# Kernel tuning notes

Hardware: AMD Instinct MI355X
Metric: run time of the kernel (lower is better)

## Reference

```python
import jax, jax.numpy as jnp
import numpy as np

# static architecture constants (match init_kwargs)
H, D, N_BASIS, MEM_LEN, QLEN = 16, 128, 1024, 512, 2048
RIDGE = 0.5
BASIS_SIGMAS = (0.005, 0.01)


def _gaussian_pdf(x, mu, sigma):
    return jnp.exp(-0.5 * ((x - mu) / sigma) ** 2) / (sigma * jnp.sqrt(2.0 * jnp.pi))


def _basis_params(n):
    # torch.meshgrid(linspace(0,1,n//2), sigmas, indexing='ij') then flatten
    m = jnp.linspace(0.0, 1.0, n // len(BASIS_SIGMAS)).astype(jnp.float32)
    mu = jnp.repeat(m, len(BASIS_SIGMAS))
    sigma = jnp.tile(jnp.asarray(BASIS_SIGMAS, jnp.float32), n // len(BASIS_SIGMAS))
    return mu, sigma


def _compute_G(l, b_mu, b_sigma, n):
    # padded linear positions on [-0.5+shift, 1.5-shift], l even -> 2l points
    shift = 1.0 / (2 * l)
    pos = jnp.linspace(-0.5 + shift, 1.5 - shift, 2 * l).astype(jnp.float32)
    F = _gaussian_pdf(pos[None, :], b_mu[:, None], b_sigma[:, None])  # [N, 2l]
    # G = F^T (F F^T + ridge I)^{-1}, then crop padding rows -> [l, N]
    G = jnp.linalg.solve(F @ F.T + RIDGE * jnp.eye(n, dtype=jnp.float32), F).T
    return G[l // 2: -(l // 2)]


def _forward(k, q, W_key, W_val, W_out, w_mu, w_sigma):
    d = H * D
    b_mu, b_sigma = _basis_params(N_BASIS)
    k = k[:, -512:, :]                                   # forward truncates memory
    l = k.shape[1]
    G = _compute_G(l, b_mu, b_sigma, N_BASIS)            # [l, N]
    # value_function: project signal onto basis coefficients B -> [1, N, d]
    B = jnp.einsum('bld,ln->bnd', k, G)
    keys = (B @ W_key.T).reshape(1, N_BASIS, H, D).transpose(0, 2, 1, 3)    # [1,H,N,D]
    values = (B @ W_val.T).reshape(1, N_BASIS, H, D).transpose(0, 2, 1, 3)  # [1,H,N,D]
    scores = jnp.einsum('bhqd,bhnd->bhqn', q / jnp.sqrt(jnp.float32(D)), keys)
    mu = jax.nn.sigmoid(scores @ w_mu)[..., None]                           # [1,H,Q,1]
    sigma_sq = jnp.maximum(jax.nn.softplus(scores @ w_sigma), 1e-4)[..., None]
    # continuous softmax over Gaussian RBFs: r_j = E_{t~N(mu,sigma_sq)}[psi_j(t)]
    # closed form: N(mu; b_mu_j, sigma_sq + b_sigma_j^2)
    r = _gaussian_pdf(b_mu, mu, jnp.sqrt(sigma_sq + b_sigma ** 2))          # [1,H,Q,N]
    context = jnp.einsum('bhqn,bhnd->bqhd', r, values).reshape(1, QLEN, d)
    return context @ W_out.T


def setup_inputs() -> dict:
    key = jax.random.key(0)
    ks = jax.random.split(key, 7)
    d = H * D
    s = 0.02
    return {
        'k': jax.random.normal(ks[0], (1, MEM_LEN, d), jnp.float32),
        'q': jax.random.normal(ks[1], (1, H, QLEN, D), jnp.float32),
        'W_key': jax.random.normal(ks[2], (d, d), jnp.float32) * s,
        'W_val': jax.random.normal(ks[3], (d, d), jnp.float32) * s,
        'W_out': jax.random.normal(ks[4], (d, d), jnp.float32) * s,
        'w_mu': jax.random.normal(ks[5], (N_BASIS,), jnp.float32) * s,
        'w_sigma': jax.random.normal(ks[6], (N_BASIS,), jnp.float32) * s,
        'new_doc': 1,
    }


def reference(k, q, W_key, W_val, W_out, w_mu, w_sigma, new_doc):
    # new_doc=True -> B_past/x_past reset, so only the fresh-memory path runs
    return _forward(k, q, W_key, W_val, W_out, w_mu, w_sigma)
```

## Files before the change

### kernel.cpp

```cpp
#include <hip/hip_runtime.h>
#include <hip/hip_bf16.h>
#include <vector>
#include <cmath>
#include <cstring>

using bf16 = __hip_bfloat16;
typedef short s16x8 __attribute__((ext_vector_type(8)));
typedef float f32x4 __attribute__((ext_vector_type(4)));

static constexpr int kH = 16, kD = 128, kNB = 1024, kML = 512, kQL = 2048, kDM = 2048;

static void compute_Gt_host(float* Gt) {
  const int n = kNB, P = 2 * kML;
  std::vector<double> F((size_t)n * P), A((size_t)n * n), pos(P);
  const double shift = 1.0 / (double)P;
  const double p0 = -0.5 + shift, p1 = 1.5 - shift;
  for (int i = 0; i < P; i++) pos[i] = p0 + (p1 - p0) * (double)i / (double)(P - 1);
  const double c0 = 0.3989422804014327;
  std::vector<int> lo(n), hi(n);
  for (int b = 0; b < n; b++) {
    double mu = (double)(b >> 1) / 511.0;
    double sg = (b & 1) ? 0.01 : 0.005;
    double c = c0 / sg;
    double* Fb = &F[(size_t)b * P];
    for (int i = 0; i < P; i++) { double t = (pos[i] - mu) / sg; Fb[i] = c * exp(-0.5 * t * t); }
    int l = 0; while (l < P - 1 && pos[l] < mu - 14.0 * sg) l++;
    int h = P - 1; while (h > 0 && pos[h] > mu + 14.0 * sg) h--;
    lo[b] = l; hi[b] = h;
  }
  for (int i = 0; i < n; i++) {
    const double* fi = &F[(size_t)i * P];
    for (int j = 0; j <= i; j++) {
      const double* fj = &F[(size_t)j * P];
      int a = lo[i] > lo[j] ? lo[i] : lo[j];
      int b2 = hi[i] < hi[j] ? hi[i] : hi[j];
      double s = 0.0;
      for (int k2 = a; k2 <= b2; k2++) s += fi[k2] * fj[k2];
      A[(size_t)i * n + j] = s;
      if (i != j) A[(size_t)j * n + i] = s;
    }
    A[(size_t)i * n + i] += 0.5;
  }
  for (int j = 0; j < n; j++) {
    double* Aj = &A[(size_t)j * n];
    double d = Aj[j];
    for (int k2 = 0; k2 < j; k2++) d -= Aj[k2] * Aj[k2];
    d = std::sqrt(d); Aj[j] = d;
    double inv = 1.0 / d;
    for (int i = j + 1; i < n; i++) {
      double* Ai = &A[(size_t)i * n];
      double s = Ai[j];
      for (int k2 = 0; k2 < j; k2++) s -= Ai[k2] * Aj[k2];
      Ai[j] = s * inv;
    }
  }
  for (int i = 0; i < n; i++) {
    double* yi = &F[(size_t)i * P];
    const double* Ai = &A[(size_t)i * n];
    for (int k2 = 0; k2 < i; k2++) {
      double lik = Ai[k2];
      const double* yk = &F[(size_t)k2 * P];
      for (int t = 0; t < P; t++) yi[t] -= lik * yk[t];
    }
    double inv = 1.0 / Ai[i];
    for (int t = 0; t < P; t++) yi[t] *= inv;
  }
  for (int i = n - 1; i >= 0; i--) {
    double* xi = &F[(size_t)i * P];
    for (int k2 = i + 1; k2 < n; k2++) {
      double lki = A[(size_t)k2 * n + i];
      const double* xk = &F[(size_t)k2 * P];
      for (int t = 0; t < P; t++) xi[t] -= lki * xk[t];
    }
    double inv = 1.0 / A[(size_t)i * n + i];
    for (int t = 0; t < P; t++) xi[t] *= inv;
  }
  for (int b = 0; b < n; b++)
    for (int l = 0; l < kML; l++)
      Gt[(size_t)b * kML + l] = (float)F[(size_t)b * P + (kML / 2) + l];
}

static unsigned short f2bf_host(float x) {
  unsigned u; std::memcpy(&u, &x, 4);
  unsigned r = (u + 0x7FFFu + ((u >> 16) & 1u)) >> 16;
  return (unsigned short)r;
}
static float bf2f_host(unsigned short b) {
  unsigned u = ((unsigned)b) << 16; float f; std::memcpy(&f, &u, 4); return f;
}

namespace {
struct Init {
  float* d_GtTf = nullptr;
  unsigned short* d_Gth = nullptr;
  unsigned short* d_Gtl = nullptr;
  float* h_GtTf_pinned = nullptr;
  unsigned short* h_Gth_pinned = nullptr;
  unsigned short* h_Gtl_pinned = nullptr;
  std::vector<float> h_GtTf;
  std::vector<unsigned short> h_Gth, h_Gtl;
  Init() {
    std::vector<float> h_Gt((size_t)kNB * kML);
    compute_Gt_host(h_Gt.data());
    h_GtTf.resize(h_Gt.size());
    h_Gth.resize(h_Gt.size());
    h_Gtl.resize(h_Gt.size());
    for (int n = 0; n < kNB; n++)
      for (int l = 0; l < kML; l++) {
        float v = h_Gt[(size_t)n * kML + l];
        h_GtTf[(size_t)l * kNB + n] = v;
        unsigned short hb = f2bf_host(v);
        h_Gth[(size_t)n * kML + l] = hb;
        h_Gtl[(size_t)n * kML + l] = f2bf_host(v - bf2f_host(hb));
      }
    const size_t fb = h_Gt.size() * 4, bb = h_Gt.size() * 2;
    if (hipMalloc((void**)&d_GtTf, fb) == hipSuccess) {
      if (hipMemcpy(d_GtTf, h_GtTf.data(), fb, hipMemcpyHostToDevice) != hipSuccess) { hipFree(d_GtTf); d_GtTf = nullptr; }
    }
    if (hipMalloc((void**)&d_Gth, bb) == hipSuccess) {
      if (hipMemcpy(d_Gth, h_Gth.data(), bb, hipMemcpyHostToDevice) != hipSuccess) { hipFree(d_Gth); d_Gth = nullptr; }
    }
    if (hipMalloc((void**)&d_Gtl, bb) == hipSuccess) {
      if (hipMemcpy(d_Gtl, h_Gtl.data(), bb, hipMemcpyHostToDevice) != hipSuccess) { hipFree(d_Gtl); d_Gtl = nullptr; }
    }
    if (!d_GtTf && hipHostMalloc((void**)&h_GtTf_pinned, fb, 0) == hipSuccess)
      std::memcpy(h_GtTf_pinned, h_GtTf.data(), fb);
    if (!d_Gth && hipHostMalloc((void**)&h_Gth_pinned, bb, 0) == hipSuccess)
      std::memcpy(h_Gth_pinned, h_Gth.data(), bb);
    if (!d_Gtl && hipHostMalloc((void**)&h_Gtl_pinned, bb, 0) == hipSuccess)
      std::memcpy(h_Gtl_pinned, h_Gtl.data(), bb);
  }
};
Init g_init;
}

__device__ inline short f2bf(float x) {
  unsigned u = __float_as_uint(x);
  unsigned r = (u + 0x7FFFu + ((u >> 16) & 1u)) >> 16;
  return (short)r;
}
__device__ inline float bf2f(short b) {
  return __uint_as_float(((unsigned)(unsigned short)b) << 16);
}

__device__ inline void gload16(const void* g, void* l) {
  __builtin_amdgcn_global_load_lds(
      (__attribute__((address_space(1))) void*)(g),
      (__attribute__((address_space(3))) void*)(l),
      16, 0, 0);
}

__global__ __launch_bounds__(256) void detect_kernel(const unsigned short* __restrict__ q,
                                                     int* __restrict__ flag) {
  int t = threadIdx.x;
  int bad = 0;
  for (int i = t; i < 4096; i += 256) {
    int e = (q[i] >> 7) & 0xFF;
    if (e >= 0x98) bad = 1;
  }
  __shared__ int s[256];
  s[t] = bad; __syncthreads();
  for (int k2 = 128; k2 > 0; k2 >>= 1) { if (t < k2) s[t] |= s[t + k2]; __syncthreads(); }
  if (t == 0) *flag = s[0];
}

__global__ __launch_bounds__(256) void conv_bf16(const void* __restrict__ in,
                                                 short* __restrict__ out, int n4,
                                                 const int* __restrict__ flag) {
  int i = blockIdx.x * 256 + threadIdx.x;
  if (i >= n4) return;
  if (*flag) {
    float4 v = ((const float4*)in)[i];
    short4 o; o.x = f2bf(v.x); o.y = f2bf(v.y); o.z = f2bf(v.z); o.w = f2bf(v.w);
    ((short4*)out)[i] = o;
  } else {
    ((short4*)out)[i] = ((const short4*)in)[i];
  }
}

__global__ __launch_bounds__(256) void gw_kernel(const float* __restrict__ GtT,
                                                 const void* __restrict__ wmu,
                                                 const void* __restrict__ wsg,
                                                 float* __restrict__ gw,
                                                 const int* __restrict__ flag) {
  const bool f32 = (*flag != 0);
  const int l = blockIdx.x, t = threadIdx.x;
  const float* row = GtT + (long long)l * kNB;
  float a = 0.f, b = 0.f;
  for (int n = t; n < kNB; n += 256) {
    float g = row[n];
    float wm_ = f32 ? ((const float*)wmu)[n] : bf2f(((const short*)wmu)[n]);
    float ws_ = f32 ? ((const float*)wsg)[n] : bf2f(((const short*)wsg)[n]);
    a += g * wm_; b += g * ws_;
  }
  __shared__ float red[2][256];
  red[0][t] = a; red[1][t] = b;
  __syncthreads();
  for (int s = 128; s > 0; s >>= 1) {
    if (t < s) { red[0][t] += red[0][t + s]; red[1][t] += red[1][t + s]; }
    __syncthreads();
  }
  if (t == 0) { gw[l] = red[0][0]; gw[kML + l] = red[1][0]; }
}

__global__ __launch_bounds__(256) void bwk_kernel(const void* __restrict__ kin,
                                                  const float* __restrict__ gw,
                                                  float* __restrict__ bw,
                                                  const int* __restrict__ flag) {
  const bool f32 = (*flag != 0);
  int j = blockIdx.x * 256 + threadIdx.x;
  int l0 = blockIdx.y * 32;
  float a = 0.f, b = 0.f;
  for (int l = l0; l < l0 + 32; l++) {
    float kv = f32 ? ((const float*)kin)[(long long)l * kDM + j]
                   : bf2f(((const short*)kin)[(long long)l * kDM + j]);
    a += kv * gw[l]; b += kv * gw[kML + l];
  }
  atomicAdd(&bw[j], a);
  atomicAdd(&bw[kDM + j], b);
}

__global__ __launch_bounds__(256) void kw_kernel(const void* __restrict__ Wk,
                                                 const float* __restrict__ bw,
                                                 float* __restrict__ kw,
                                                 const int* __restrict__ flag) {
  const bool f32 = (*flag != 0);
  int i = blockIdx.x;
  float smu = 0.f, ssg = 0.f;
  if (f32) {
    const float* row = (const float*)Wk + (long long)i * kDM;
    for (int j = threadIdx.x; j < kDM; j += 256) { float w = row[j]; smu += w * bw[j]; ssg += w * bw[kDM + j]; }
  } else {
    const short* row = (const short*)Wk + (long long)i * kDM;
    for (int j = threadIdx.x; j < kDM; j += 256) { float w = bf2f(row[j]); smu += w * bw[j]; ssg += w * bw[kDM + j]; }
  }
  __shared__ float red[2][256];
  red[0][threadIdx.x] = smu; red[1][threadIdx.x] = ssg;
  __syncthreads();
  for (int s = 128; s > 0; s >>= 1) {
    if (threadIdx.x < (unsigned)s) {
      red[0][threadIdx.x] += red[0][threadIdx.x + s];
      red[1][threadIdx.x] += red[1][threadIdx.x + s];
    }
    __syncthreads();
  }
  if (threadIdx.x == 0) { kw[i] = red[0][0]; kw[kDM + i] = red[1][0]; }
}

__global__ __launch_bounds__(256) void musig_kernel(const void* __restrict__ q,
                                                    const float* __restrict__ kw,
                                                    float* __restrict__ mu,
                                                    float* __restrict__ sigsq,
                                                    const int* __restrict__ flag) {
  const bool f32 = (*flag != 0);
  int w = threadIdx.x >> 6, lane = threadIdx.x & 63;
  int idx = blockIdx.x * 4 + w;
  int h = idx >> 11;
  const float* kmu = kw + h * kD;
  const float* ksg = kw + kDM + h * kD;
  float q0, q1;
  if (f32) {
    const float* qrow = (const float*)q + (long long)idx * kD;
    q0 = qrow[lane]; q1 = qrow[lane + 64];
  } else {
    const short* qrow = (const short*)q + (long long)idx * kD;
    q0 = bf2f(qrow[lane]); q1 = bf2f(qrow[lane + 64]);
  }
  float a = q0 * kmu[lane] + q1 * kmu[lane + 64];
  float b = q0 * ksg[lane] + q1 * ksg[lane + 64];
  for (int s = 32; s > 0; s >>= 1) { a += __shfl_xor(a, s); b += __shfl_xor(b, s); }
  if (lane == 0) {
    const float inv_sqrt_d = 0.08838834764831845f;
    float zm = a * inv_sqrt_d, zs = b * inv_sqrt_d;
    mu[idx] = 1.f / (1.f + __expf(-zm));
    float sp = (zs > 20.f) ? zs : log1pf(__expf(zs));
    sigsq[idx] = fmaxf(sp, 1e-4f);
  }
}

template <int CSTORE>
__global__ __launch_bounds__(256) void mfma_gemm_bt(
    const short* __restrict__ A0, int lda, long long sA,
    const short* __restrict__ BT0, int ldb, long long sB,
    void* __restrict__ C0, int ldc, long long sC,
    int K, const int* __restrict__ flag) {
  __shared__ s16x8 lA[2][1024];
  __shared__ s16x8 lB[2][512];
  const short* A = A0 + (long long)blockIdx.z * sA;
  const short* BT = BT0 + (long long)blockIdx.z * sB;
  const int t = threadIdx.x;
  const int wave = t >> 6, lane = t & 63;
  const int quad = lane >> 4, l16 = lane & 15;
  const int wm = wave >> 1, wn = wave & 1;
  const int m0 = blockIdx.y * 128, n0 = blockIdx.x * 64;
  const int srow = lane & 15, skc = lane >> 4;
  auto stage = [&](int b, int kk) {
#pragma unroll
    for (int i = 0; i < 2; i++) {
      int sub = wave + i * 4;
      int m = sub * 16 + srow;
#pragma unroll
      for (int ks = 0; ks < 2; ks++)
        gload16(A + (long long)(m0 + m) * lda + kk + ks * 32 + skc * 8,
                &lA[b][ks * 512 + sub * 64]);
    }
    int mB = wave * 16 + srow;
#pragma unroll
    for (int ks = 0; ks < 2; ks++)
      gload16(BT + (long long)(n0 + mB) * ldb + kk + ks * 32 + skc * 8,
              &lB[b][ks * 256 + wave * 64]);
  };
  f32x4 acc[4][2];
  const f32x4 z = {0.f, 0.f, 0.f, 0.f};
#pragma unroll
  for (int i = 0; i < 4; i++)
#pragma unroll
    for (int j = 0; j < 2; j++) acc[i][j] = z;
  stage(0, 0);
  __syncthreads();
  int cur = 0;
  for (int k0 = 0; k0 < K; k0 += 64) {
    if (k0 + 64 < K) stage(cur ^ 1, k0 + 64);
#pragma unroll
    for (int ks = 0; ks < 2; ks++) {
      s16x8 af[4], bfr[2];
#pragma unroll
      for (int i = 0; i < 4; i++) af[i] = lA[cur][ks * 512 + (wm * 4 + i) * 64 + lane];
#pragma unroll
      for (int j = 0; j < 2; j++) bfr[j] = lB[cur][ks * 256 + (wn * 2 + j) * 64 + lane];
#pragma unroll
      for (int i = 0; i < 4; i++)
#pragma unroll
        for (int j = 0; j < 2; j++)
          acc[i][j] = __builtin_amdgcn_mfma_f32_16x16x32_bf16(af[i], bfr[j], acc[i][j], 0, 0, 0);
    }
    __syncthreads();
    cur ^= 1;
  }
  if (CSTORE == 0) {
    short* Cp = (short*)C0 + (long long)blockIdx.z * sC;
#pragma unroll
    for (int i = 0; i < 4; i++)
#pragma unroll
      for (int j = 0; j < 2; j++) {
        int gn = n0 + (wn * 2 + j) * 16 + l16;
#pragma unroll
        for (int rg = 0; rg < 4; rg++) {
          int gm = m0 + (wm * 4 + i) * 16 + quad * 4 + rg;
          Cp[(long long)gm * ldc + gn] = f2bf(acc[i][j][rg]);
        }
      }
  } else {
    if (*flag) {
      float* Cp = (float*)C0 + (long long)blockIdx.z * sC;
#pragma unroll
      for (int i = 0; i < 4; i++)
#pragma unroll
        for (int j = 0; j < 2; j++) {
          int gn = n0 + (wn * 2 + j) * 16 + l16;
#pragma unroll
          for (int rg = 0; rg < 4; rg++) {
            int gm = m0 + (wm * 4 + i) * 16 + quad * 4 + rg;
            Cp[(long long)gm * ldc + gn] = acc[i][j][rg];
          }
        }
    } else {
      short* Cp = (short*)C0 + (long long)blockIdx.z * sC;
#pragma unroll
      for (int i = 0; i < 4; i++)
#pragma unroll
        for (int j = 0; j < 2; j++) {
          int gn = n0 + (wn * 2 + j) * 16 + l16;
#pragma unroll
          for (int rg = 0; rg < 4; rg++) {
            int gm = m0 + (wm * 4 + i) * 16 + quad * 4 + rg;
            Cp[(long long)gm * ldc + gn] = f2bf(acc[i][j][rg]);
          }
        }
    }
  }
}

__global__ __launch_bounds__(256) void mfma_gemm_sk(
    const short* __restrict__ A0, int lda,
    const short* __restrict__ BT0, int ldb,
    float* __restrict__ P, int ldc) {
  __shared__ s16x8 lA[2][1024], lB[2][512];
  const int t = threadIdx.x;
  const int wave = t >> 6, lane = t & 63;
  const int quad = lane >> 4, l16 = lane & 15;
  const int wm = wave >> 1, wn = wave & 1;
  const int m0 = blockIdx.y * 128, n0 = blockIdx.x * 64;
  const int kbeg = blockIdx.z * 512, kend = kbeg + 512;
  const int srow = lane & 15, skc = lane >> 4;
  auto stage = [&](int b, int kk) {
#pragma unroll
    for (int i = 0; i < 2; i++) {
      int sub = wave + i * 4;
      int m = sub * 16 + srow;
#pragma unroll
      for (int ks = 0; ks < 2; ks++)
        gload16(A0 + (long long)(m0 + m) * lda + kk + ks * 32 + skc * 8,
                &lA[b][ks * 512 + sub * 64]);
    }
    int mB = wave * 16 + srow;
#pragma unroll
    for (int ks = 0; ks < 2; ks++)
      gload16(BT0 + (long long)(n0 + mB) * ldb + kk + ks * 32 + skc * 8,
              &lB[b][ks * 256 + wave * 64]);
  };
  f32x4 acc[4][2];
  const f32x4 z = {0.f, 0.f, 0.f, 0.f};
#pragma unroll
  for (int i = 0; i < 4; i++)
#pragma unroll
    for (int j = 0; j < 2; j++) acc[i][j] = z;
  stage(0, kbeg);
  __syncthreads();
  int cur = 0;
  for (int k0 = kbeg; k0 < kend; k0 += 64) {
    if (k0 + 64 < kend) stage(cur ^ 1, k0 + 64);
#pragma unroll
    for (int ks = 0; ks < 2; ks++) {
      s16x8 af[4], bfr[2];
#pragma unroll
      for (int i = 0; i < 4; i++) af[i] = lA[cur][ks * 512 + (wm * 4 + i) * 64 + lane];
#pragma unroll
      for (int j = 0; j < 2; j++) bfr[j] = lB[cur][ks * 256 + (wn * 2 + j) * 64 + lane];
#pragma unroll
      for (int i = 0; i < 4; i++)
#pragma unroll
        for (int j = 0; j < 2; j++)
          acc[i][j] = __builtin_amdgcn_mfma_f32_16x16x32_bf16(af[i], bfr[j], acc[i][j], 0, 0, 0);
    }
    __syncthreads();
    cur ^= 1;
  }
  float* Cp = P + (long long)blockIdx.z * kML * kDM;
#pragma unroll
  for (int i = 0; i < 4; i++)
#pragma unroll
    for (int j = 0; j < 2; j++) {
      int gn = n0 + (wn * 2 + j) * 16 + l16;
#pragma unroll
      for (int rg = 0; rg < 4; rg++) {
        int gm = m0 + (wm * 4 + i) * 16 + quad * 4 + rg;
        Cp[(long long)gm * ldc + gn] = acc[i][j][rg];
      }
    }
}

__global__ __launch_bounds__(256) void reduceT_kernel(const float* __restrict__ P,
                                                      short* __restrict__ kvT) {
  __shared__ float tile[64][65];
  const int bd = blockIdx.x, bl = blockIdx.y;
  const int tx = threadIdx.x & 63, ty = threadIdx.x >> 6;
  for (int i = ty; i < 64; i += 4) {
    int l = bl * 64 + i, d = bd * 64 + tx;
    float s = 0.f;
#pragma unroll
    for (int z = 0; z < 4; z++) s += P[((long long)z * kML + l) * kDM + d];
    tile[i][tx] = s;
  }
  __syncthreads();
  for (int i = ty; i < 64; i += 4) {
    int d = bd * 64 + i, l = bl * 64 + tx;
    kvT[(long long)d * kML + l] = f2bf(tile[tx][i]);
  }
}

__global__ __launch_bounds__(256) void mfma_gemm_bt2(
    const short* __restrict__ A0, int lda,
    const short* __restrict__ BTh, const short* __restrict__ BTl, int ldb,
    short* __restrict__ Ch, short* __restrict__ Cl, int ldc, int K) {
  __shared__ s16x8 lA[2][256], lBh[2][256], lBl[2][256];
  const int t = threadIdx.x;
  const int wave = t >> 6, lane = t & 63;
  const int quad = lane >> 4, l16 = lane & 15;
  const int wm = wave >> 1, wn = wave & 1;
  const int m0 = blockIdx.y * 64, n0 = blockIdx.x * 64;
  const int srow = lane & 15, skc = lane >> 4;
  auto stage = [&](int b, int kk) {
    int m = wave * 16 + srow;
    gload16(A0 + (long long)(m0 + m) * lda + kk + skc * 8, &lA[b][wave * 64]);
    gload16(BTh + (long long)(n0 + m) * ldb + kk + skc * 8, &lBh[b][wave * 64]);
    gload16(BTl + (long long)(n0 + m) * ldb + kk + skc * 8, &lBl[b][wave * 64]);
  };
  f32x4 acc[2][2];
  const f32x4 z = {0.f, 0.f, 0.f, 0.f};
#pragma unroll
  for (int i = 0; i < 2; i++)
#pragma unroll
    for (int j = 0; j < 2; j++) acc[i][j] = z;
  stage(0, 0);
  __syncthreads();
  int cur = 0;
  for (int k0 = 0; k0 < K; k0 += 32) {
    if (k0 + 32 < K) stage(cur ^ 1, k0 + 32);
    s16x8 af[2], bh[2], bl[2];
#pragma unroll
    for (int i = 0; i < 2; i++) af[i] = lA[cur][(wm * 2 + i) * 64 + lane];
#pragma unroll
    for (int j = 0; j < 2; j++) {
      bh[j] = lBh[cur][(wn * 2 + j) * 64 + lane];
      bl[j] = lBl[cur][(wn * 2 + j) * 64 + lane];
    }
#pragma unroll
    for (int i = 0; i < 2; i++)
#pragma unroll
      for (int j = 0; j < 2; j++) {
        acc[i][j] = __builtin_amdgcn_mfma_f32_16x16x32_bf16(af[i], bh[j], acc[i][j], 0, 0, 0);
        acc[i][j] = __builtin_amdgcn_mfma_f32_16x16x32_bf16(af[i], bl[j], acc[i][j], 0, 0, 0);
      }
    __syncthreads();
    cur ^= 1;
  }
#pragma unroll
  for (int i = 0; i < 2; i++)
#pragma unroll
    for (int j = 0; j < 2; j++) {
      int gn = n0 + (wn * 2 + j) * 16 + l16;
#pragma unroll
      for (int rg = 0; rg < 4; rg++) {
        int gm = m0 + (wm * 2 + i) * 16 + quad * 4 + rg;
        float v = acc[i][j][rg];
        short hb = f2bf(v);
        Ch[(long long)gm * ldc + gn] = hb;
        Cl[(long long)gm * ldc + gn] = f2bf(v - bf2f(hb));
      }
    }
}

__global__ __launch_bounds__(256) void mfma_rv(
    const float* __restrict__ mu_all, const float* __restrict__ s2_all,
    const short* __restrict__ VTh, const short* __restrict__ VTl,
    short* __restrict__ ctx) {
  __shared__ s16x8 lAh[2][256], lAl[2][256], lBh[2][512], lBl[2][512];
  const int t = threadIdx.x;
  const int wave = t >> 6, lane = t & 63;
  const int quad = lane >> 4, l16 = lane & 15;
  const int wm = wave >> 1, wn = wave & 1;
  const int h = blockIdx.z;
  const int m0 = blockIdx.y * 64;
  const int r0 = t >> 2, kc = t & 3;
  const int srow = lane & 15, skc = lane >> 4;
  const long long voff = (long long)h * kD * kNB;
  const int row = h * kQL + m0 + r0;
  const float m_ = mu_all[row], s2 = s2_all[row];
  float ivs[2], cof[2];
  ivs[0] = rsqrtf(s2 + 2.5e-5f);
  ivs[1] = rsqrtf(s2 + 1e-4f);
  cof[0] = 0.3989422804014327f * ivs[0];
  cof[1] = 0.3989422804014327f * ivs[1];
  const int cidx = (r0 >> 4) * 64 + kc * 16 + (r0 & 15);
  auto stageB = [&](int b, int kk) {
#pragma unroll
    for (int i = 0; i < 2; i++) {
      int sub = wave + i * 4;
      int m = sub * 16 + srow;
      gload16(VTh + voff + (long long)m * kNB + kk + skc * 8, &lBh[b][sub * 64]);
      gload16(VTl + voff + (long long)m * kNB + kk + skc * 8, &lBl[b][sub * 64]);
    }
  };
  auto stageA = [&](int b, int kk) {
    s16x8 hv, lv;
#pragma unroll
    for (int jj = 0; jj < 8; jj++) {
      int n = kk + kc * 8 + jj;
      float bmu = (float)(n >> 1) * (1.f / 511.f);
      int p = jj & 1;
      float tt = (bmu - m_) * ivs[p];
      float v = cof[p] * __expf(-0.5f * tt * tt);
      short hb = f2bf(v);
      hv[jj] = hb;
      lv[jj] = f2bf(v - bf2f(hb));
    }
    lAh[b][cidx] = hv;
    lAl[b][cidx] = lv;
  };
  f32x4 acc[2][4];
  const f32x4 z = {0.f, 0.f, 0.f, 0.f};
#pragma unroll
  for (int i = 0; i < 2; i++)
#pragma unroll
    for (int j = 0; j < 4; j++) acc[i][j] = z;
  stageB(0, 0);
  stageA(0, 0);
  __syncthreads();
  int cur = 0;
  for (int k0 = 0; k0 < kNB; k0 += 32) {
    if (k0 + 32 < kNB) {
      stageB(cur ^ 1, k0 + 32);
      stageA(cur ^ 1, k0 + 32);
    }
    s16x8 ah[2], al[2], bh[4], bl[4];
#pragma unroll
    for (int i = 0; i < 2; i++) {
      ah[i] = lAh[cur][(wm * 2 + i) * 64 + lane];
      al[i] = lAl[cur][(wm * 2 + i) * 64 + lane];
    }
#pragma unroll
    for (int j = 0; j < 4; j++) {
      bh[j] = lBh[cur][(wn * 4 + j) * 64 + lane];
      bl[j] = lBl[cur][(wn * 4 + j) * 64 + lane];
    }
#pragma unroll
    for (int i = 0; i < 2; i++)
#pragma unroll
      for (int j = 0; j < 4; j++) {
        acc[i][j] = __builtin_amdgcn_mfma_f32_16x16x32_bf16(ah[i], bh[j], acc[i][j], 0, 0, 0);
        acc[i][j] = __builtin_amdgcn_mfma_f32_16x16x32_bf16(ah[i], bl[j], acc[i][j], 0, 0, 0);
        acc[i][j] = __builtin_amdgcn_mfma_f32_16x16x32_bf16(al[i], bh[j], acc[i][j], 0, 0, 0);
      }
    __syncthreads();
    cur ^= 1;
  }
  short* Cp = ctx + h * kD;
#pragma unroll
  for (int i = 0; i < 2; i++)
#pragma unroll
    for (int j = 0; j < 4; j++) {
      int gn = (wn * 4 + j) * 16 + l16;
#pragma unroll
      for (int rg = 0; rg < 4; rg++) {
        int gm = m0 + (wm * 2 + i) * 16 + quad * 4 + rg;
        Cp[(long long)gm * kDM + gn] = f2bf(acc[i][j][rg]);
      }
    }
}

extern "C" void kernel_launch(void* const* d_in, const int* in_sizes, int n_in,
                              void* d_out, int out_size, void* d_ws, size_t ws_size,
                              hipStream_t stream) {
  (void)in_sizes; (void)n_in; (void)out_size; (void)ws_size;
  const void* kmem = d_in[0];
  const void* q    = d_in[1];
  const void* Wk   = d_in[2];
  const void* Wv   = d_in[3];
  const void* Wo   = d_in[4];
  const void* wmu  = d_in[5];
  const void* wsg  = d_in[6];

  char* ws = (char*)d_ws;
  short* k_bf  = (short*)ws;
  short* kvT   = (short*)(ws + ((size_t)2 << 20));
  short* Wv_bf = (short*)(ws + ((size_t)4 << 20));
  short* Wo_bf = Wv_bf;
  float* Pbuf  = (float*)(ws + ((size_t)12 << 20));
  short* VTh   = (short*)(ws + ((size_t)12 << 20));
  short* VTl   = (short*)(ws + ((size_t)16 << 20));
  short* ctx   = (short*)(ws + ((size_t)20 << 20));
  float* tail  = (float*)(ws + ((size_t)28 << 20));
  float* gw    = tail;
  float* bw    = gw + 2 * kML;
  float* kw    = bw + 2 * kDM;
  float* mu    = kw + 2 * kDM;
  float* sigsq = mu + kH * kQL;
  int*   flag  = (int*)(sigsq + kH * kQL);
  float* gtffall = (float*)(ws + ((size_t)28 << 20) + ((size_t)1 << 19));
  short* ghfall  = (short*)(ws + ((size_t)30 << 20) + ((size_t)1 << 19));
  short* glfall  = (short*)(ws + ((size_t)31 << 20) + ((size_t)1 << 19));

  const float* GtTf = g_init.d_GtTf;
  if (!GtTf) {
    const void* src = g_init.h_GtTf_pinned ? (const void*)g_init.h_GtTf_pinned
                                           : (const void*)g_init.h_GtTf.data();
    hipMemcpyAsync(gtffall, src, (size_t)kNB * kML * 4, hipMemcpyHostToDevice, stream);
    GtTf = gtffall;
  }
  const short* Gh = (const short*)g_init.d_Gth;
  if (!Gh) {
    const void* src = g_init.h_Gth_pinned ? (const void*)g_init.h_Gth_pinned
                                          : (const void*)g_init.h_Gth.data();
    hipMemcpyAsync(ghfall, src, (size_t)kNB * kML * 2, hipMemcpyHostToDevice, stream);
    Gh = ghfall;
  }
  const short* Gl = (const short*)g_init.d_Gtl;
  if (!Gl) {
    const void* src = g_init.h_Gtl_pinned ? (const void*)g_init.h_Gtl_pinned
                                          : (const void*)g_init.h_Gtl.data();
    hipMemcpyAsync(glfall, src, (size_t)kNB * kML * 2, hipMemcpyHostToDevice, stream);
    Gl = glfall;
  }

  detect_kernel<<<1, 256, 0, stream>>>((const unsigned short*)q, flag);

  conv_bf16<<<(kML * kDM / 4 + 255) / 256, 256, 0, stream>>>(kmem, k_bf, kML * kDM / 4, flag);
  conv_bf16<<<(kDM * kDM / 4 + 255) / 256, 256, 0, stream>>>(Wv, Wv_bf, kDM * kDM / 4, flag);

  gw_kernel<<<kML, 256, 0, stream>>>(GtTf, wmu, wsg, gw, flag);
  hipMemsetAsync(bw, 0, 2 * kDM * sizeof(float), stream);
  bwk_kernel<<<dim3(kDM / 256, kML / 32), 256, 0, stream>>>(kmem, gw, bw, flag);
  kw_kernel<<<kDM, 256, 0, stream>>>(Wk, bw, kw, flag);
  musig_kernel<<<kH * kQL / 4, 256, 0, stream>>>(q, kw, mu, sigsq, flag);

  mfma_gemm_sk<<<dim3(kDM / 64, kML / 128, 4), 256, 0, stream>>>(
      k_bf, kDM, Wv_bf, kDM, Pbuf, kDM);
  reduceT_kernel<<<dim3(kDM / 64, kML / 64), 256, 0, stream>>>(Pbuf, kvT);

  conv_bf16<<<(kDM * kDM / 4 + 255) / 256, 256, 0, stream>>>(Wo, Wo_bf, kDM * kDM / 4, flag);

  mfma_gemm_bt2<<<dim3(kNB / 64, kDM / 64, 1), 256, 0, stream>>>(
      kvT, kML, Gh, Gl, kML, VTh, VTl, kNB, kML);

  mfma_rv<<<dim3(1, kQL / 64, kH), 256, 0, stream>>>(mu, sigsq, VTh, VTl, ctx);

  mfma_gemm_bt<2><<<dim3(kDM / 64, kQL / 128, 1), 256, 0, stream>>>(
      ctx, kDM, 0, Wo_bf, kDM, 0, d_out, kDM, 0, kDM, flag);
}
```

Measured before the change: 273.1 us.

## Triple-buffer LDS staging in all MFMA GEMM kernels with partial vmcnt waits

Moves the four MFMA GEMM kernels from double to triple LDS buffering, with two tiles prefetched ahead. The full __syncthreads is replaced by s_waitcnt vmcnt(N) plus a barrier, so loads for the next-next tile stay in flight while the current tile computes. This is meant to hide global-to-LDS latency better. It costs 50% more LDS per block, which may lower occupancy, and it depends on hand-counted vmcnt values matching the number of async loads each stage issues.

Result: no change. 269.5 us (-1.3%).

```diff
diff --git a/kernel.cpp b/kernel.cpp
--- a/kernel.cpp
+++ b/kernel.cpp
@@ -9,6 +9,13 @@
 typedef float f32x4 __attribute__((ext_vector_type(4)));
 
 static constexpr int kH = 16, kD = 128, kNB = 1024, kML = 512, kQL = 2048, kDM = 2048;
+
+#define VMB(N) do { asm volatile("s_waitcnt vmcnt(" #N ")" ::: "memory"); \
+                    __builtin_amdgcn_s_barrier(); \
+                    asm volatile("" ::: "memory"); } while (0)
+#define VMLB(N) do { asm volatile("s_waitcnt vmcnt(" #N ") lgkmcnt(0)" ::: "memory"); \
+                     __builtin_amdgcn_s_barrier(); \
+                     asm volatile("" ::: "memory"); } while (0)
 
 static void compute_Gt_host(float* Gt) {
   const int n = kNB, P = 2 * kML;
@@ -284,8 +291,8 @@
     const short* __restrict__ BT0, int ldb, long long sB,
     void* __restrict__ C0, int ldc, long long sC,
     int K, const int* __restrict__ flag) {
-  __shared__ s16x8 lA[2][1024];
-  __shared__ s16x8 lB[2][512];
+  __shared__ s16x8 lA[3][1024];
+  __shared__ s16x8 lB[3][512];
   const short* A = A0 + (long long)blockIdx.z * sA;
   const short* BT = BT0 + (long long)blockIdx.z * sB;
   const int t = threadIdx.x;
@@ -317,10 +324,13 @@
 #pragma unroll
     for (int j = 0; j < 2; j++) acc[i][j] = z;
   stage(0, 0);
-  __syncthreads();
-  int cur = 0;
-  for (int k0 = 0; k0 < K; k0 += 64) {
-    if (k0 + 64 < K) stage(cur ^ 1, k0 + 64);
+  stage(1, 64);
+  VMB(6);
+  const int NT = K >> 6;
+  int cur = 0, pf = 2;
+  for (int tt = 0; tt < NT; ++tt) {
+    const bool more = (tt + 2 < NT);
+    if (more) stage(pf, (tt + 2) << 6);
 #pragma unroll
     for (int ks = 0; ks < 2; ks++) {
       s16x8 af[4], bfr[2];
@@ -334,8 +344,9 @@
         for (int j = 0; j < 2; j++)
           acc[i][j] = __builtin_amdgcn_mfma_f32_16x16x32_bf16(af[i], bfr[j], acc[i][j], 0, 0, 0);
     }
-    __syncthreads();
-    cur ^= 1;
+    if (more) VMB(6); else VMB(0);
+    cur = (cur == 2) ? 0 : cur + 1;
+    pf = (pf == 2) ? 0 : pf + 1;
   }
   if (CSTORE == 0) {
     short* Cp = (short*)C0 + (long long)blockIdx.z * sC;
@@ -385,13 +396,13 @@
     const short* __restrict__ A0, int lda,
     const short* __restrict__ BT0, int ldb,
     float* __restrict__ P, int ldc) {
-  __shared__ s16x8 lA[2][1024], lB[2][512];
+  __shared__ s16x8 lA[3][1024], lB[3][512];
   const int t = threadIdx.x;
   const int wave = t >> 6, lane = t & 63;
   const int quad = lane >> 4, l16 = lane & 15;
   const int wm = wave >> 1, wn = wave & 1;
   const int m0 = blockIdx.y * 128, n0 = blockIdx.x * 64;
-  const int kbeg = blockIdx.z * 512, kend = kbeg + 512;
+  const int kbeg = blockIdx.z * 512;
   const int srow = lane & 15, skc = lane >> 4;
   auto stage = [&](int b, int kk) {
 #pragma unroll
@@ -416,10 +427,13 @@
 #pragma unroll
     for (int j = 0; j < 2; j++) acc[i][j] = z;
   stage(0, kbeg);
-  __syncthreads();
-  int cur = 0;
-  for (int k0 = kbeg; k0 < kend; k0 += 64) {
-    if (k0 + 64 < kend) stage(cur ^ 1, k0 + 64);
+  stage(1, kbeg + 64);
+  VMB(6);
+  const int NT = 8;
+  int cur = 0, pf = 2;
+  for (int tt = 0; tt < NT; ++tt) {
+    const bool more = (tt + 2 < NT);
+    if (more) stage(pf, kbeg + ((tt + 2) << 6));
 #pragma unroll
     for (int ks = 0; ks < 2; ks++) {
       s16x8 af[4], bfr[2];
@@ -433,8 +447,9 @@
         for (int j = 0; j < 2; j++)
           acc[i][j] = __builtin_amdgcn_mfma_f32_16x16x32_bf16(af[i], bfr[j], acc[i][j], 0, 0, 0);
     }
-    __syncthreads();
-    cur ^= 1;
+    if (more) VMB(6); else VMB(0);
+    cur = (cur == 2) ? 0 : cur + 1;
+    pf = (pf == 2) ? 0 : pf + 1;
   }
   float* Cp = P + (long long)blockIdx.z * kML * kDM;
 #pragma unroll
@@ -473,7 +488,7 @@
     const short* __restrict__ A0, int lda,
     const short* __restrict__ BTh, const short* __restrict__ BTl, int ldb,
     short* __restrict__ Ch, short* __restrict__ Cl, int ldc, int K) {
-  __shared__ s16x8 lA[2][256], lBh[2][256], lBl[2][256];
+  __shared__ s16x8 lA[3][256], lBh[3][256], lBl[3][256];
   const int t = threadIdx.x;
   const int wave = t >> 6, lane = t & 63;
   const int quad = lane >> 4, l16 = lane & 15;
@@ -493,10 +508,13 @@
 #pragma unroll
     for (int j = 0; j < 2; j++) acc[i][j] = z;
   stage(0, 0);
-  __syncthreads();
-  int cur = 0;
-  for (int k0 = 0; k0 < K; k0 += 32) {
-    if (k0 + 32 < K) stage(cur ^ 1, k0 + 32);
+  stage(1, 32);
+  VMB(3);
+  const int NT = K >> 5;
+  int cur = 0, pf = 2;
+  for (int tt = 0; tt < NT; ++tt) {
+    const bool more = (tt + 2 < NT);
+    if (more) stage(pf, (tt + 2) << 5);
     s16x8 af[2], bh[2], bl[2];
 #pragma unroll
     for (int i = 0; i < 2; i++) af[i] = lA[cur][(wm * 2 + i) * 64 + lane];
@@ -512,8 +530,9 @@
         acc[i][j] = __builtin_amdgcn_mfma_f32_16x16x32_bf16(af[i], bh[j], acc[i][j], 0, 0, 0);
         acc[i][j] = __builtin_amdgcn_mfma_f32_16x16x32_bf16(af[i], bl[j], acc[i][j], 0, 0, 0);
       }
-    __syncthreads();
-    cur ^= 1;
+    if (more) VMB(3); else VMB(0);
+    cur = (cur == 2) ? 0 : cur + 1;
+    pf = (pf == 2) ? 0 : pf + 1;
   }
 #pragma unroll
   for (int i = 0; i < 2; i++)
@@ -535,7 +554,7 @@
     const float* __restrict__ mu_all, const float* __restrict__ s2_all,
     const short* __restrict__ VTh, const short* __restrict__ VTl,
     short* __restrict__ ctx) {
-  __shared__ s16x8 lAh[2][256], lAl[2][256], lBh[2][512], lBl[2][512];
+  __shared__ s16x8 lAh[3][256], lAl[3][256], lBh[3][512], lBl[3][512];
   const int t = threadIdx.x;
   const int wave = t >> 6, lane = t & 63;
   const int quad = lane >> 4, l16 = lane & 15;
@@ -586,12 +605,16 @@
     for (int j = 0; j < 4; j++) acc[i][j] = z;
   stageB(0, 0);
   stageA(0, 0);
-  __syncthreads();
-  int cur = 0;
-  for (int k0 = 0; k0 < kNB; k0 += 32) {
-    if (k0 + 32 < kNB) {
-      stageB(cur ^ 1, k0 + 32);
-      stageA(cur ^ 1, k0 + 32);
+  stageB(1, 32);
+  stageA(1, 32);
+  VMLB(4);
+  const int NT = kNB >> 5;
+  int cur = 0, pf = 2;
+  for (int tt = 0; tt < NT; ++tt) {
+    const bool more = (tt + 2 < NT);
+    if (more) {
+      stageB(pf, (tt + 2) << 5);
+      stageA(pf, (tt + 2) << 5);
     }
     s16x8 ah[2], al[2], bh[4], bl[4];
 #pragma unroll
@@ -612,8 +635,9 @@
         acc[i][j] = __builtin_amdgcn_mfma_f32_16x16x32_bf16(ah[i], bl[j], acc[i][j], 0, 0, 0);
         acc[i][j] = __builtin_amdgcn_mfma_f32_16x16x32_bf16(al[i], bh[j], acc[i][j], 0, 0, 0);
       }
-    __syncthreads();
-    cur ^= 1;
+    if (more) VMLB(4); else VMLB(0);
+    cur = (cur == 2) ? 0 : cur + 1;
+    pf = (pf == 2) ? 0 : pf + 1;
   }
   short* Cp = ctx + h * kD;
 #pragma unroll
```
